# Optimization experiments

Hardware: AMD Instinct MI355X
Metric: run time of the kernel (lower is better)

## Reference

```python
import jax, jax.numpy as jnp
import numpy as np


def setup_inputs() -> dict:
    key = jax.random.key(0)
    k1, k2 = jax.random.split(key)
    T, D, E = 8192, 4096, 64  # tokens, model_dim, num_experts
    x = jax.random.normal(k1, (T, D), dtype=jnp.float32)
    wg = jax.random.normal(k2, (E, D), dtype=jnp.float32) * (1.0 / np.sqrt(D))
    return {"x": x, "wg": wg}


def reference(x, wg):
    # gate logits: nn.Linear(model_dim, num_experts, bias=False) in fp32
    logits = jnp.einsum('td,ed->te', x.astype(jnp.float32), wg)  # [T, E]
    gates = jax.nn.softmax(logits, axis=1)                        # [T, E]
    # top1gating (eval mode: no noise): argmax over gates
    indices1_s = jnp.argmax(gates, axis=1)                        # [T] int
    # gates = (gates * one_hot(indices1_s)).sum(dim=1) == gather of the max gate
    gates1_s = jnp.take_along_axis(gates, indices1_s[:, None], axis=1)[:, 0]  # [T]
    return indices1_s, gates1_s
```

## Files before the change

### kernel.cpp

```cpp
#include <hip/hip_runtime.h>

typedef __attribute__((ext_vector_type(8))) short bf16x8;
typedef __attribute__((ext_vector_type(4))) float f32x4;
typedef __attribute__((ext_vector_type(4))) unsigned u32x4;

constexpr int TN = 8192;
constexpr int DN = 4096;
constexpr int EN = 64;

constexpr int BM = 32;
constexpr int NS = DN / 32;
constexpr int NT = 16;

__device__ __forceinline__ unsigned short f2bf(float f) {
    unsigned u = __builtin_bit_cast(unsigned, f);
    u += 0x7FFFu + ((u >> 16) & 1u);
    return (unsigned short)(u >> 16);
}
__device__ __forceinline__ float bf2f(unsigned short h) {
    unsigned u = ((unsigned)h) << 16;
    return __builtin_bit_cast(float, u);
}

__device__ __forceinline__ void split_pair(float f0, float f1,
                                           unsigned& hi, unsigned& lo) {
    unsigned u0 = __builtin_bit_cast(unsigned, f0);
    unsigned u1 = __builtin_bit_cast(unsigned, f1);
    unsigned r0 = u0 + 0x7FFFu + ((u0 >> 16) & 1u);
    unsigned r1 = u1 + 0x7FFFu + ((u1 >> 16) & 1u);
    hi = __builtin_amdgcn_perm(r1, r0, 0x07060302u);
    float h0 = __builtin_bit_cast(float, r0 & 0xFFFF0000u);
    float h1 = __builtin_bit_cast(float, r1 & 0xFFFF0000u);
    unsigned v0 = __builtin_bit_cast(unsigned, f0 - h0);
    unsigned v1 = __builtin_bit_cast(unsigned, f1 - h1);
    unsigned s0 = v0 + 0x7FFFu + ((v0 >> 16) & 1u);
    unsigned s1 = v1 + 0x7FFFu + ((v1 >> 16) & 1u);
    lo = __builtin_amdgcn_perm(s1, s0, 0x07060302u);
}

__global__ __launch_bounds__(256)
void wg_frag_kernel(const float* __restrict__ wg, unsigned short* __restrict__ BF) {
    const int gid = blockIdx.x * 256 + threadIdx.x;
    const int l  = gid & 63;
    const int et = (gid >> 6) & 3;
    const int s  = (gid >> 8) & (NS - 1);
    const int p  = gid >> 15;
    const int e  = et * 16 + (l & 15);
    const int k  = s * 32 + (l >> 4) * 8;

    const float* src = wg + (size_t)e * DN + k;
    float4 v0 = *reinterpret_cast<const float4*>(src);
    float4 v1 = *reinterpret_cast<const float4*>(src + 4);
    float f[8] = {v0.x, v0.y, v0.z, v0.w, v1.x, v1.y, v1.z, v1.w};
    unsigned short o[8];
#pragma unroll
    for (int j = 0; j < 8; ++j) {
        unsigned short h = f2bf(f[j]);
        o[j] = p ? f2bf(f[j] - bf2f(h)) : h;
    }
    unsigned short* dst = BF + (((size_t)p * NS + s) * 4 + et) * 512 + (size_t)l * 8;
    *reinterpret_cast<ushort4*>(dst)     = make_ushort4(o[0], o[1], o[2], o[3]);
    *reinterpret_cast<ushort4*>(dst + 4) = make_ushort4(o[4], o[5], o[6], o[7]);
}

__global__ __launch_bounds__(512, 2)
void gate_fused_kernel(const float* __restrict__ x,
                       const unsigned short* __restrict__ BF,
                       float* __restrict__ out) {
    __shared__ float L[8][BM][68];

    const int tid  = threadIdx.x;
    const int lane = tid & 63;
    const int w    = tid >> 6;
    const int kq   = w & 3;
    const int kh   = w >> 2;
    const int r0   = blockIdx.x * BM;

    const int fr  = lane & 15;
    const int fko = (lane >> 4) * 8;

    const float* xa = x + (size_t)(r0 + fr) * DN + fko;

    f32x4 acc[2][4] = {};

    float4 XA[3][2][2];
    bf16x8 Bq[2][8];

    auto loadA = [&](int set, int t) {
        const int s = kh * 64 + t * 4 + kq;
        const float* p = xa + (size_t)s * 32;
#pragma unroll
        for (int rh = 0; rh < 2; ++rh) {
            const float* pr = p + (size_t)rh * 16 * DN;
            XA[set][rh][0] = *reinterpret_cast<const float4*>(pr);
            XA[set][rh][1] = *reinterpret_cast<const float4*>(pr + 4);
        }
    };
    auto loadB = [&](int set, int t) {
        const int s = kh * 64 + t * 4 + kq;
        const unsigned short* bp = BF + (size_t)s * 2048 + (size_t)lane * 8;
#pragma unroll
        for (int et = 0; et < 4; ++et)
            Bq[set][et] = *reinterpret_cast<const bf16x8*>(bp + et * 512);
#pragma unroll
        for (int et = 0; et < 4; ++et)
            Bq[set][4 + et] = *reinterpret_cast<const bf16x8*>(bp + (size_t)NS * 2048 + et * 512);
    };
    auto compute = [&](int aset, int bset) {
        bf16x8 ah[2], al[2];
#pragma unroll
        for (int rh = 0; rh < 2; ++rh) {
            float f[8] = {XA[aset][rh][0].x, XA[aset][rh][0].y,
                          XA[aset][rh][0].z, XA[aset][rh][0].w,
                          XA[aset][rh][1].x, XA[aset][rh][1].y,
                          XA[aset][rh][1].z, XA[aset][rh][1].w};
            u32x4 uh, ul;
#pragma unroll
            for (int q = 0; q < 4; ++q) {
                unsigned hw, lw;
                split_pair(f[2 * q], f[2 * q + 1], hw, lw);
                uh[q] = hw; ul[q] = lw;
            }
            ah[rh] = __builtin_bit_cast(bf16x8, uh);
            al[rh] = __builtin_bit_cast(bf16x8, ul);
        }
#pragma unroll
        for (int et = 0; et < 4; ++et)
#pragma unroll
            for (int rh = 0; rh < 2; ++rh)
                acc[rh][et] = __builtin_amdgcn_mfma_f32_16x16x32_bf16(ah[rh], Bq[bset][et], acc[rh][et], 0, 0, 0);
#pragma unroll
        for (int et = 0; et < 4; ++et)
#pragma unroll
            for (int rh = 0; rh < 2; ++rh)
                acc[rh][et] = __builtin_amdgcn_mfma_f32_16x16x32_bf16(al[rh], Bq[bset][et], acc[rh][et], 0, 0, 0);
#pragma unroll
        for (int et = 0; et < 4; ++et)
#pragma unroll
            for (int rh = 0; rh < 2; ++rh)
                acc[rh][et] = __builtin_amdgcn_mfma_f32_16x16x32_bf16(ah[rh], Bq[bset][4 + et], acc[rh][et], 0, 0, 0);
#pragma unroll
        for (int et = 0; et < 4; ++et)
#pragma unroll
            for (int rh = 0; rh < 2; ++rh)
                acc[rh][et] = __builtin_amdgcn_mfma_f32_16x16x32_bf16(al[rh], Bq[bset][4 + et], acc[rh][et], 0, 0, 0);
    };

    loadB(0, 0);
    loadA(0, 0);
    loadB(1, 1);
    loadA(1, 1);
    loadA(2, 2);
#pragma unroll
    for (int t = 0; t < NT; ++t) {
        compute(t % 3, t & 1);
        if (t + 2 < NT) loadB(t & 1, t + 2);
        if (t + 3 < NT) loadA(t % 3, t + 3);
        asm volatile("" ::: "memory");
    }

#pragma unroll
    for (int rh = 0; rh < 2; ++rh)
#pragma unroll
        for (int et = 0; et < 4; ++et)
#pragma unroll
            for (int r = 0; r < 4; ++r)
                L[w][rh * 16 + (lane >> 4) * 4 + r][et * 16 + fr] = acc[rh][et][r];
    __syncthreads();

    {
        const int row = tid >> 4;
        const int eg  = tid & 15;
        float v[4];
#pragma unroll
        for (int j = 0; j < 4; ++j) {
            float s = L[0][row][eg * 4 + j];
#pragma unroll
            for (int q = 1; q < 8; ++q) s += L[q][row][eg * 4 + j];
            v[j] = s;
        }
        float m = v[0];
        int idx = eg * 4;
#pragma unroll
        for (int j = 1; j < 4; ++j)
            if (v[j] > m) { m = v[j]; idx = eg * 4 + j; }
#pragma unroll
        for (int d = 1; d < 16; d <<= 1) {
            float om = __shfl_xor(m, d);
            int   oi = __shfl_xor(idx, d);
            if (om > m || (om == m && oi < idx)) { m = om; idx = oi; }
        }
        float s = 0.0f;
#pragma unroll
        for (int j = 0; j < 4; ++j) s += __expf(v[j] - m);
#pragma unroll
        for (int d = 1; d < 16; d <<= 1) s += __shfl_xor(s, d);
        if (eg == 0) {
            out[r0 + row]      = (float)idx;
            out[TN + r0 + row] = 1.0f / s;
        }
    }
}

extern "C" void kernel_launch(void* const* d_in, const int* in_sizes, int n_in,
                              void* d_out, int out_size, void* d_ws, size_t ws_size,
                              hipStream_t stream) {
    const float* x  = (const float*)d_in[0];
    const float* wg = (const float*)d_in[1];
    float* out = (float*)d_out;

    unsigned short* BF = (unsigned short*)d_ws;

    wg_frag_kernel<<<dim3(256), dim3(256), 0, stream>>>(wg, BF);
    gate_fused_kernel<<<dim3(TN / BM), dim3(512), 0, stream>>>(x, BF, out);
}
```

Measured before the change: 38.94 us.

## Split-K gate GEMM with LDS-staged weights and separate top1 softmax kernel

Restructures the gate GEMM to a split-K layout. Each block takes 512 rows and one sixteenth of K and stages its bf16 hi/lo weight fragments in LDS once. Each wave then computes a 64x64 tile reading B from LDS instead of re-reading it from global memory per 32-row tile. Partial sums go to a workspace buffer and a new kernel reduces the 16 partials and does the argmax/softmax. The cost is an extra kernel launch plus writing and reading 16 x 8192 x 64 fp32 partials (about 32 MB each way) in exchange for much higher weight reuse.

```diff
diff --git a/kernel.cpp b/kernel.cpp
--- a/kernel.cpp
+++ b/kernel.cpp
@@ -2,15 +2,16 @@
 
 typedef __attribute__((ext_vector_type(8))) short bf16x8;
 typedef __attribute__((ext_vector_type(4))) float f32x4;
-typedef __attribute__((ext_vector_type(4))) unsigned u32x4;
 
 constexpr int TN = 8192;
 constexpr int DN = 4096;
 constexpr int EN = 64;
 
-constexpr int BM = 32;
-constexpr int NS = DN / 32;
-constexpr int NT = 16;
+constexpr int NS     = DN / 32;
+constexpr int KSPLIT = 16;
+constexpr int SLOTS  = NS / KSPLIT;
+constexpr int RB     = 512;
+constexpr int RW     = 64;
 
 __device__ __forceinline__ unsigned short f2bf(float f) {
     unsigned u = __builtin_bit_cast(unsigned, f);
@@ -21,7 +22,6 @@
     unsigned u = ((unsigned)h) << 16;
     return __builtin_bit_cast(float, u);
 }
-
 __device__ __forceinline__ void split_pair(float f0, float f1,
                                            unsigned& hi, unsigned& lo) {
     unsigned u0 = __builtin_bit_cast(unsigned, f0);
@@ -64,141 +64,146 @@
 }
 
 __global__ __launch_bounds__(512, 2)
-void gate_fused_kernel(const float* __restrict__ x,
-                       const unsigned short* __restrict__ BF,
-                       float* __restrict__ out) {
-    __shared__ float L[8][BM][68];
+void gate_gemm_kernel(const float* __restrict__ x,
+                      const unsigned short* __restrict__ BF,
+                      float* __restrict__ part) {
+    __shared__ uint4 LB[SLOTS * 512];
 
     const int tid  = threadIdx.x;
     const int lane = tid & 63;
     const int w    = tid >> 6;
-    const int kq   = w & 3;
-    const int kh   = w >> 2;
-    const int r0   = blockIdx.x * BM;
-
-    const int fr  = lane & 15;
-    const int fko = (lane >> 4) * 8;
-
-    const float* xa = x + (size_t)(r0 + fr) * DN + fko;
-
-    f32x4 acc[2][4] = {};
-
-    float4 XA[3][2][2];
-    bf16x8 Bq[2][8];
+    const int rt   = blockIdx.x >> 4;
+    const int ks   = blockIdx.x & 15;
+    const int r0   = rt * RB;
+
+    const int fr = lane & 15;
+    const int g  = lane >> 4;
+    const int fko = g * 8;
+
+    {
+        const uint4* gh = reinterpret_cast<const uint4*>(BF);
+        const uint4* gl = gh + 32768;
+#pragma unroll
+        for (int i = 0; i < 8; ++i) {
+            int e = tid + i * 512;
+            int slot = e >> 9, plane = (e >> 8) & 1, off = e & 255;
+            int gidx = (ks * SLOTS + slot) * 256 + off;
+            LB[e] = plane ? gl[gidx] : gh[gidx];
+        }
+    }
+    __syncthreads();
+
+    const float* xa = x + (size_t)(r0 + w * RW + fr) * DN + fko;
+
+    f32x4 acc[4][4] = {};
+    float4 XA[2][4][2];
 
     auto loadA = [&](int set, int t) {
-        const int s = kh * 64 + t * 4 + kq;
-        const float* p = xa + (size_t)s * 32;
-#pragma unroll
-        for (int rh = 0; rh < 2; ++rh) {
+        const float* p = xa + (size_t)(ks * SLOTS + t) * 32;
+#pragma unroll
+        for (int rh = 0; rh < 4; ++rh) {
             const float* pr = p + (size_t)rh * 16 * DN;
             XA[set][rh][0] = *reinterpret_cast<const float4*>(pr);
             XA[set][rh][1] = *reinterpret_cast<const float4*>(pr + 4);
         }
     };
-    auto loadB = [&](int set, int t) {
-        const int s = kh * 64 + t * 4 + kq;
-        const unsigned short* bp = BF + (size_t)s * 2048 + (size_t)lane * 8;
-#pragma unroll
-        for (int et = 0; et < 4; ++et)
-            Bq[set][et] = *reinterpret_cast<const bf16x8*>(bp + et * 512);
-#pragma unroll
-        for (int et = 0; et < 4; ++et)
-            Bq[set][4 + et] = *reinterpret_cast<const bf16x8*>(bp + (size_t)NS * 2048 + et * 512);
+    auto compute = [&](int set, int t) {
+        bf16x8 bh[4], bl[4];
+#pragma unroll
+        for (int et = 0; et < 4; ++et) {
+            bh[et] = __builtin_bit_cast(bf16x8, LB[t * 512 + et * 64 + lane]);
+            bl[et] = __builtin_bit_cast(bf16x8, LB[t * 512 + 256 + et * 64 + lane]);
+        }
+        bf16x8 ah[4], al[4];
+#pragma unroll
+        for (int rh = 0; rh < 4; ++rh) {
+            float f[8] = {XA[set][rh][0].x, XA[set][rh][0].y,
+                          XA[set][rh][0].z, XA[set][rh][0].w,
+                          XA[set][rh][1].x, XA[set][rh][1].y,
+                          XA[set][rh][1].z, XA[set][rh][1].w};
+            unsigned uh[4], ul[4];
+#pragma unroll
+            for (int q = 0; q < 4; ++q)
+                split_pair(f[2 * q], f[2 * q + 1], uh[q], ul[q]);
+            uint4 vh = make_uint4(uh[0], uh[1], uh[2], uh[3]);
+            uint4 vl = make_uint4(ul[0], ul[1], ul[2], ul[3]);
+            ah[rh] = __builtin_bit_cast(bf16x8, vh);
+            al[rh] = __builtin_bit_cast(bf16x8, vl);
+        }
+#pragma unroll
+        for (int et = 0; et < 4; ++et)
+#pragma unroll
+            for (int rh = 0; rh < 4; ++rh)
+                acc[rh][et] = __builtin_amdgcn_mfma_f32_16x16x32_bf16(ah[rh], bh[et], acc[rh][et], 0, 0, 0);
+#pragma unroll
+        for (int et = 0; et < 4; ++et)
+#pragma unroll
+            for (int rh = 0; rh < 4; ++rh)
+                acc[rh][et] = __builtin_amdgcn_mfma_f32_16x16x32_bf16(al[rh], bh[et], acc[rh][et], 0, 0, 0);
+#pragma unroll
+        for (int et = 0; et < 4; ++et)
+#pragma unroll
+            for (int rh = 0; rh < 4; ++rh)
+                acc[rh][et] = __builtin_amdgcn_mfma_f32_16x16x32_bf16(ah[rh], bl[et], acc[rh][et], 0, 0, 0);
+#pragma unroll
+        for (int et = 0; et < 4; ++et)
+#pragma unroll
+            for (int rh = 0; rh < 4; ++rh)
+                acc[rh][et] = __builtin_amdgcn_mfma_f32_16x16x32_bf16(al[rh], bl[et], acc[rh][et], 0, 0, 0);
     };
-    auto compute = [&](int aset, int bset) {
-        bf16x8 ah[2], al[2];
-#pragma unroll
-        for (int rh = 0; rh < 2; ++rh) {
-            float f[8] = {XA[aset][rh][0].x, XA[aset][rh][0].y,
-                          XA[aset][rh][0].z, XA[aset][rh][0].w,
-                          XA[aset][rh][1].x, XA[aset][rh][1].y,
-                          XA[aset][rh][1].z, XA[aset][rh][1].w};
-            u32x4 uh, ul;
-#pragma unroll
-            for (int q = 0; q < 4; ++q) {
-                unsigned hw, lw;
-                split_pair(f[2 * q], f[2 * q + 1], hw, lw);
-                uh[q] = hw; ul[q] = lw;
-            }
-            ah[rh] = __builtin_bit_cast(bf16x8, uh);
-            al[rh] = __builtin_bit_cast(bf16x8, ul);
-        }
-#pragma unroll
-        for (int et = 0; et < 4; ++et)
-#pragma unroll
-            for (int rh = 0; rh < 2; ++rh)
-                acc[rh][et] = __builtin_amdgcn_mfma_f32_16x16x32_bf16(ah[rh], Bq[bset][et], acc[rh][et], 0, 0, 0);
-#pragma unroll
-        for (int et = 0; et < 4; ++et)
-#pragma unroll
-            for (int rh = 0; rh < 2; ++rh)
-                acc[rh][et] = __builtin_amdgcn_mfma_f32_16x16x32_bf16(al[rh], Bq[bset][et], acc[rh][et], 0, 0, 0);
-#pragma unroll
-        for (int et = 0; et < 4; ++et)
-#pragma unroll
-            for (int rh = 0; rh < 2; ++rh)
-                acc[rh][et] = __builtin_amdgcn_mfma_f32_16x16x32_bf16(ah[rh], Bq[bset][4 + et], acc[rh][et], 0, 0, 0);
-#pragma unroll
-        for (int et = 0; et < 4; ++et)
-#pragma unroll
-            for (int rh = 0; rh < 2; ++rh)
-                acc[rh][et] = __builtin_amdgcn_mfma_f32_16x16x32_bf16(al[rh], Bq[bset][4 + et], acc[rh][et], 0, 0, 0);
-    };
-
-    loadB(0, 0);
+
     loadA(0, 0);
-    loadB(1, 1);
     loadA(1, 1);
-    loadA(2, 2);
-#pragma unroll
-    for (int t = 0; t < NT; ++t) {
-        compute(t % 3, t & 1);
-        if (t + 2 < NT) loadB(t & 1, t + 2);
-        if (t + 3 < NT) loadA(t % 3, t + 3);
+#pragma unroll
+    for (int t = 0; t < SLOTS; ++t) {
+        compute(t & 1, t);
+        if (t + 2 < SLOTS) loadA(t & 1, t + 2);
         asm volatile("" ::: "memory");
     }
 
-#pragma unroll
-    for (int rh = 0; rh < 2; ++rh)
+    float* dst = part + ((size_t)ks * TN + r0 + w * RW) * EN;
+#pragma unroll
+    for (int rh = 0; rh < 4; ++rh)
 #pragma unroll
         for (int et = 0; et < 4; ++et)
 #pragma unroll
             for (int r = 0; r < 4; ++r)
-                L[w][rh * 16 + (lane >> 4) * 4 + r][et * 16 + fr] = acc[rh][et][r];
-    __syncthreads();
-
-    {
-        const int row = tid >> 4;
-        const int eg  = tid & 15;
-        float v[4];
-#pragma unroll
-        for (int j = 0; j < 4; ++j) {
-            float s = L[0][row][eg * 4 + j];
-#pragma unroll
-            for (int q = 1; q < 8; ++q) s += L[q][row][eg * 4 + j];
-            v[j] = s;
-        }
-        float m = v[0];
-        int idx = eg * 4;
-#pragma unroll
-        for (int j = 1; j < 4; ++j)
-            if (v[j] > m) { m = v[j]; idx = eg * 4 + j; }
-#pragma unroll
-        for (int d = 1; d < 16; d <<= 1) {
-            float om = __shfl_xor(m, d);
-            int   oi = __shfl_xor(idx, d);
-            if (om > m || (om == m && oi < idx)) { m = om; idx = oi; }
-        }
-        float s = 0.0f;
-#pragma unroll
-        for (int j = 0; j < 4; ++j) s += __expf(v[j] - m);
-#pragma unroll
-        for (int d = 1; d < 16; d <<= 1) s += __shfl_xor(s, d);
-        if (eg == 0) {
-            out[r0 + row]      = (float)idx;
-            out[TN + r0 + row] = 1.0f / s;
-        }
+                dst[(size_t)(rh * 16 + g * 4 + r) * EN + et * 16 + fr] = acc[rh][et][r];
+}
+
+__global__ __launch_bounds__(256)
+void top1_softmax_kernel(const float* __restrict__ part, float* __restrict__ out) {
+    const int gid = blockIdx.x * blockDim.x + threadIdx.x;
+    const int row = gid >> 4;
+    const int eg  = gid & 15;
+    if (row >= TN) return;
+
+    float v[4] = {};
+#pragma unroll
+    for (int h = 0; h < KSPLIT; ++h) {
+        float4 t = *reinterpret_cast<const float4*>(
+            &part[((size_t)h * TN + row) * EN + eg * 4]);
+        v[0] += t.x; v[1] += t.y; v[2] += t.z; v[3] += t.w;
+    }
+    float m = v[0];
+    int idx = eg * 4;
+#pragma unroll
+    for (int j = 1; j < 4; ++j)
+        if (v[j] > m) { m = v[j]; idx = eg * 4 + j; }
+#pragma unroll
+    for (int d = 1; d < 16; d <<= 1) {
+        float om = __shfl_xor(m, d);
+        int   oi = __shfl_xor(idx, d);
+        if (om > m || (om == m && oi < idx)) { m = om; idx = oi; }
+    }
+    float s = 0.0f;
+#pragma unroll
+    for (int j = 0; j < 4; ++j) s += __expf(v[j] - m);
+#pragma unroll
+    for (int d = 1; d < 16; d <<= 1) s += __shfl_xor(s, d);
+    if (eg == 0) {
+        out[row]      = (float)idx;
+        out[TN + row] = 1.0f / s;
     }
 }
 
@@ -209,8 +214,11 @@
     const float* wg = (const float*)d_in[1];
     float* out = (float*)d_out;
 
+    constexpr size_t BF_BYTES = (size_t)2 * NS * 4 * 512 * 2;
     unsigned short* BF = (unsigned short*)d_ws;
+    float* part = (float*)((char*)d_ws + BF_BYTES);
 
     wg_frag_kernel<<<dim3(256), dim3(256), 0, stream>>>(wg, BF);
-    gate_fused_kernel<<<dim3(TN / BM), dim3(512), 0, stream>>>(x, BF, out);
-}
+    gate_gemm_kernel<<<dim3((TN / RB) * KSPLIT), dim3(512), 0, stream>>>(x, BF, part);
+    top1_softmax_kernel<<<dim3(TN * 16 / 256), dim3(256), 0, stream>>>(part, out);
+}
```

Measured after the change: 42.75 us. 1.1x slower.
